# Kernel tuning notes

Measured on AMD Instinct MI355X. Metric: run time of the kernel, lower is better.

Reference implementation:

```python
import jax, jax.numpy as jnp
import numpy as np

N = 50000       # nodes
E = 800000      # edges (before self-loops)
F_IN = 128
HID = 64
HEADS = 4
OUT_DIM = 128
N_CLS = 2
NG = 500        # num graphs
SLOPE = 0.2     # GATConv leaky_relu negative slope
EPS = 1e-5      # BatchNorm eps


def setup_inputs() -> dict:
    key = jax.random.key(0)
    ks = jax.random.split(key, 24)
    s = 0.05
    d = {
        "x": jax.random.normal(ks[0], (N, F_IN), jnp.float32),
        "edge_index": jax.random.randint(ks[1], (2, E), 0, N, jnp.int64),
        "batch": jnp.sort(jax.random.randint(ks[2], (N,), 0, NG, jnp.int64)),
        # GATConv 1
        "W1": jax.random.normal(ks[3], (F_IN, HEADS * HID), jnp.float32) * s,
        "att_src1": jax.random.normal(ks[4], (HEADS, HID), jnp.float32) * s,
        "att_dst1": jax.random.normal(ks[5], (HEADS, HID), jnp.float32) * s,
        "b1": jnp.zeros((HEADS * HID,), jnp.float32),
        # BN1 (eval mode)
        "g1": jnp.ones((HEADS * HID,), jnp.float32),
        "be1": jnp.zeros((HEADS * HID,), jnp.float32),
        "rm1": jnp.zeros((HEADS * HID,), jnp.float32),
        "rv1": jnp.ones((HEADS * HID,), jnp.float32),
        # GATConv 2
        "W2": jax.random.normal(ks[6], (HEADS * HID, HEADS * HID), jnp.float32) * s,
        "att_src2": jax.random.normal(ks[7], (HEADS, HID), jnp.float32) * s,
        "att_dst2": jax.random.normal(ks[8], (HEADS, HID), jnp.float32) * s,
        "b2": jnp.zeros((HEADS * HID,), jnp.float32),
        # BN2 (eval mode)
        "g2": jnp.ones((HEADS * HID,), jnp.float32),
        "be2": jnp.zeros((HEADS * HID,), jnp.float32),
        "rm2": jnp.zeros((HEADS * HID,), jnp.float32),
        "rv2": jnp.ones((HEADS * HID,), jnp.float32),
        # MLP head
        "lw1": jax.random.normal(ks[9], (HEADS * HID, OUT_DIM), jnp.float32) * s,
        "lb1": jnp.zeros((OUT_DIM,), jnp.float32),
        "lw2": jax.random.normal(ks[10], (OUT_DIM, N_CLS), jnp.float32) * s,
        "lb2": jnp.zeros((N_CLS,), jnp.float32),
    }
    return d


def _gat_conv(x, src, dst, W, a_src, a_dst, b):
    """PyG GATConv (concat heads, add_self_loops=True, eval -> no dropout)."""
    n = x.shape[0]
    h = (x @ W).reshape(n, HEADS, -1)            # [N, H, C]
    loop = jnp.arange(n)
    s = jnp.concatenate([src, loop])             # self-loops appended
    d = jnp.concatenate([dst, loop])
    a_s = jnp.sum(h * a_src, axis=-1)            # [N, H]
    a_d = jnp.sum(h * a_dst, axis=-1)            # [N, H]
    e = jax.nn.leaky_relu(a_s[s] + a_d[d], SLOPE)   # [Et, H]
    # softmax over incoming edges per destination node
    m = jax.ops.segment_max(e, d, num_segments=n)
    ex = jnp.exp(e - m[d])
    denom = jax.ops.segment_sum(ex, d, num_segments=n)
    alpha = ex / denom[d]                        # [Et, H]
    msg = h[s] * alpha[:, :, None]               # [Et, H, C]
    out = jax.ops.segment_sum(msg, d, num_segments=n)
    return out.reshape(n, -1) + b


def _bn_eval(x, g, be, rm, rv):
    return (x - rm) * jax.lax.rsqrt(rv + EPS) * g + be


def reference(x, edge_index, batch, W1, att_src1, att_dst1, b1, g1, be1, rm1, rv1,
              W2, att_src2, att_dst2, b2, g2, be2, rm2, rv2, lw1, lb1, lw2, lb2):
    src, dst = edge_index[0], edge_index[1]
    h = jax.nn.relu(_gat_conv(x, src, dst, W1, att_src1, att_dst1, b1))
    h = _bn_eval(h, g1, be1, rm1, rv1)
    h = jax.nn.relu(_gat_conv(h, src, dst, W2, att_src2, att_dst2, b2))
    h = _bn_eval(h, g2, be2, rm2, rv2)
    # global mean pool over graphs
    sums = jax.ops.segment_sum(h, batch, num_segments=NG)
    cnt = jax.ops.segment_sum(jnp.ones((h.shape[0],), h.dtype), batch, num_segments=NG)
    pooled = sums / jnp.clip(cnt, 1.0)[:, None]
    z = jax.nn.relu(pooled @ lw1 + lb1)
    return z @ lw2 + lb2
```

## Files before the change

kernel.cpp:

```cpp
#include <hip/hip_runtime.h>
#include <hip/hip_bf16.h>
#include <math.h>

#define N_NODES 50000
#define M_PAD   50048
#define N_EDGES 800000
#define F_IN 128
#define HID 64
#define HEADS 4
#define FEAT 256
#define OUT_DIM 128
#define N_CLS 2
#define NG 500
#define SLOPE 0.2f
#define BN_EPS 1e-5f
#define WCAP 64
#define NCHUNK ((N_NODES + 255) / 256)

typedef __attribute__((ext_vector_type(8))) short short8;
typedef __attribute__((ext_vector_type(4))) float floatx4;
typedef __attribute__((ext_vector_type(2))) float floatx2;

__device__ inline unsigned short f2bf(float f) {
    unsigned int u = __float_as_uint(f);
    unsigned int lsb = (u >> 16) & 1u;
    return (unsigned short)((u + 0x7fffu + lsb) >> 16);
}

template<bool AF32>
__global__ __launch_bounds__(256, 2) void gemm_mfma_gat(
    const void* __restrict__ Av, const unsigned short* __restrict__ BT,
    const float* __restrict__ att_src, const float* __restrict__ att_dst,
    unsigned char* __restrict__ h8, float* __restrict__ a_s,
    float* __restrict__ a_d, int K) {
    constexpr int LS = 40;
    constexpr int C8 = 272;
    __shared__ __align__(16) unsigned char smem_raw[128 * C8];
    unsigned short* As = (unsigned short*)smem_raw;
    unsigned short* Bs = As + 128 * LS;
    unsigned char*  s8 = smem_raw;
    int t = threadIdx.x;
    int lane = t & 63, w = t >> 6;
    int row0 = blockIdx.x * 128;
    int mrow = lane & 15, quad = lane >> 4;

    floatx4 acc[8][4] = {};

    int rA = t >> 2, cA = (t & 3) * 8;

    const unsigned short* Ab = (const unsigned short*)Av;
    const float* Af = (const float*)Av;

    for (int k0 = 0; k0 < K; k0 += 32) {
        #pragma unroll
        for (int j = 0; j < 2; j++) {
            int r = rA + j * 64;
            if (AF32) {
                uint4 pk = make_uint4(0, 0, 0, 0);
                if (row0 + r < N_NODES) {
                    float4 f0 = *(const float4*)&Af[(long long)(row0 + r) * K + k0 + cA];
                    float4 f1 = *(const float4*)&Af[(long long)(row0 + r) * K + k0 + cA + 4];
                    pk.x = (unsigned)f2bf(f0.x) | ((unsigned)f2bf(f0.y) << 16);
                    pk.y = (unsigned)f2bf(f0.z) | ((unsigned)f2bf(f0.w) << 16);
                    pk.z = (unsigned)f2bf(f1.x) | ((unsigned)f2bf(f1.y) << 16);
                    pk.w = (unsigned)f2bf(f1.z) | ((unsigned)f2bf(f1.w) << 16);
                }
                *(uint4*)&As[r * LS + cA] = pk;
            } else {
                *(uint4*)&As[r * LS + cA] = *(const uint4*)&Ab[(long long)(row0 + r) * K + k0 + cA];
            }
        }
        #pragma unroll
        for (int j = 0; j < 4; j++) {
            int r = rA + j * 64;
            *(uint4*)&Bs[r * LS + cA] = *(const uint4*)&BT[(long long)r * K + k0 + cA];
        }
        __syncthreads();
        short8 bf[4];
        #pragma unroll
        for (int ni = 0; ni < 4; ni++)
            bf[ni] = *(const short8*)&Bs[(w * 64 + ni * 16 + mrow) * LS + quad * 8];
        #pragma unroll
        for (int mi = 0; mi < 8; mi++) {
            short8 af = *(const short8*)&As[(mi * 16 + mrow) * LS + quad * 8];
            #pragma unroll
            for (int ni = 0; ni < 4; ni++)
                acc[mi][ni] = __builtin_amdgcn_mfma_f32_16x16x32_bf16(af, bf[ni],
                                                                      acc[mi][ni], 0, 0, 0);
        }
        __syncthreads();
    }

    float ats[4], atd[4];
    #pragma unroll
    for (int ni = 0; ni < 4; ni++) {
        ats[ni] = att_src[w * 64 + ni * 16 + mrow];
        atd[ni] = att_dst[w * 64 + ni * 16 + mrow];
    }
    #pragma unroll
    for (int mi = 0; mi < 8; mi++) {
        #pragma unroll
        for (int r = 0; r < 4; r++) {
            int row = row0 + mi * 16 + quad * 4 + r;
            float ps = 0.f, pd = 0.f;
            #pragma unroll
            for (int ni = 0; ni < 4; ni++) {
                float v = acc[mi][ni][r];
                ps += v * ats[ni];
                pd += v * atd[ni];
            }
            #pragma unroll
            for (int off = 1; off < 16; off <<= 1) {
                ps += __shfl_xor(ps, off);
                pd += __shfl_xor(pd, off);
            }
            if (mrow == 0 && row < N_NODES) {
                a_s[row * 4 + w] = ps;
                a_d[row * 4 + w] = pd;
            }
        }
    }

    #pragma unroll
    for (int mi = 0; mi < 8; mi++)
        #pragma unroll
        for (int r = 0; r < 4; r++) {
            int row = mi * 16 + quad * 4 + r;
            #pragma unroll
            for (int ni = 0; ni < 4; ni += 2) {
                int pk = __builtin_amdgcn_cvt_pk_fp8_f32(acc[mi][ni][r],
                                                         acc[mi][ni + 1][r], 0, false);
                s8[row * C8 + w * 64 + ni * 16 + mrow]       = (unsigned char)(pk & 0xff);
                s8[row * C8 + w * 64 + (ni + 1) * 16 + mrow] = (unsigned char)((pk >> 8) & 0xff);
            }
        }
    __syncthreads();
    {
        int r2 = t >> 1, half = t & 1;
        const uint4* sp = (const uint4*)&s8[r2 * C8 + half * 128];
        uint4* dp = (uint4*)&h8[(long long)(row0 + r2) * FEAT + half * 128];
        #pragma unroll
        for (int k = 0; k < 8; k++)
            dp[k] = sp[k];
    }
}

__global__ void prep(const float* __restrict__ W1, const float* __restrict__ W2,
                     unsigned short* __restrict__ W1T, unsigned short* __restrict__ W2T,
                     int* __restrict__ deg, unsigned long long* __restrict__ h1bf_pad) {
    int i = blockIdx.x * 256 + threadIdx.x;
    if (i < F_IN * 256) {
        int k = i >> 8, n = i & 255;
        W1T[n * F_IN + k] = f2bf(W1[i]);
    }
    int j = i - F_IN * 256;
    if (j >= 0 && j < FEAT * 256) {
        int k = j >> 8, n = j & 255;
        W2T[n * FEAT + k] = f2bf(W2[j]);
    }
    if (i < N_NODES) deg[i] = 0;
    if (i < (M_PAD - N_NODES) * FEAT / 4) h1bf_pad[i] = 0ULL;
}

__global__ void degree_count(const int* __restrict__ src, const int* __restrict__ dst,
                             int* __restrict__ deg, int* __restrict__ epos) {
    int e = blockIdx.x * blockDim.x + threadIdx.x;
    if (e >= N_EDGES + N_NODES) return;
    int d = (e < N_EDGES) ? dst[e] : (e - N_EDGES);
    epos[e] = atomicAdd(&deg[d], 1);
}

__global__ __launch_bounds__(256) void scan_k1(const int* __restrict__ deg,
                                               int* __restrict__ bsum) {
    int b = blockIdx.x, t = threadIdx.x;
    int i = b * 256 + t;
    int v = (i < N_NODES) ? deg[i] : 0;
    #pragma unroll
    for (int off = 32; off > 0; off >>= 1) v += __shfl_down(v, off);
    __shared__ int ws[4];
    if ((t & 63) == 0) ws[t >> 6] = v;
    __syncthreads();
    if (t == 0) bsum[b] = ws[0] + ws[1] + ws[2] + ws[3];
}

__global__ __launch_bounds__(256) void scan_k2(const int* __restrict__ bsum,
                                               int* __restrict__ boff,
                                               int* __restrict__ row_start) {
    int t = threadIdx.x;
    int lane = t & 63, wid = t >> 6;
    int v = (t < NCHUNK) ? bsum[t] : 0;
    int x = v;
    #pragma unroll
    for (int off = 1; off < 64; off <<= 1) {
        int y = __shfl_up(x, off);
        if (lane >= off) x += y;
    }
    __shared__ int wsum[4], woff[4];
    if (lane == 63) wsum[wid] = x;
    __syncthreads();
    if (t == 0) {
        int s = 0;
        #pragma unroll
        for (int w = 0; w < 4; w++) { int tw = wsum[w]; woff[w] = s; s += tw; }
        row_start[N_NODES] = s;
    }
    __syncthreads();
    if (t < NCHUNK) boff[t] = x - v + woff[wid];
}

__global__ __launch_bounds__(256) void scan_k3(const int* __restrict__ deg,
                                               const int* __restrict__ boff,
                                               int* __restrict__ row_start) {
    int b = blockIdx.x, t = threadIdx.x;
    int lane = t & 63, wid = t >> 6;
    int i = b * 256 + t;
    int v = (i < N_NODES) ? deg[i] : 0;
    int x = v;
    #pragma unroll
    for (int off = 1; off < 64; off <<= 1) {
        int y = __shfl_up(x, off);
        if (lane >= off) x += y;
    }
    __shared__ int wsum[4], woff[4];
    if (lane == 63) wsum[wid] = x;
    __syncthreads();
    if (t == 0) {
        int s = boff[b];
        #pragma unroll
        for (int w = 0; w < 4; w++) { int tw = wsum[w]; woff[w] = s; s += tw; }
    }
    __syncthreads();
    if (i < N_NODES) row_start[i] = x - v + woff[wid];
}

__global__ void scatter_edges(const int* __restrict__ src, const int* __restrict__ dst,
                              const int* __restrict__ row_start, const int* __restrict__ epos,
                              int* __restrict__ csr_src) {
    int e = blockIdx.x * blockDim.x + threadIdx.x;
    if (e >= N_EDGES + N_NODES) return;
    int s, d;
    if (e < N_EDGES) { s = src[e]; d = dst[e]; } else { s = d = e - N_EDGES; }
    csr_src[row_start[d] + epos[e]] = s;
}

__global__ __launch_bounds__(256) void gat_fused(
    const int* __restrict__ row_start, const int* __restrict__ csr_src,
    const float* __restrict__ a_s, const float* __restrict__ a_d,
    const unsigned char* __restrict__ h8, const float* __restrict__ bias,
    const float* __restrict__ g, const float* __restrict__ be,
    const float* __restrict__ rm, const float* __restrict__ rv,
    unsigned short* __restrict__ out16) {
    int t = threadIdx.x;
    int lane = t & 63;
    int w = t >> 6;
    int hd = lane >> 4;
    int d = blockIdx.x * 4 + w;

    __shared__ float p_lds[4 * WCAP * 4];
    __shared__ int   o_lds[4 * WCAP];
    float* pw = &p_lds[w * WCAP * 4];
    int*   ow = &o_lds[w * WCAP];

    const unsigned int* __restrict__ H1 = (const unsigned int*)h8;

    int rs = row_start[d], re = row_start[d + 1];
    int deg = re - rs;
    float4 ad4 = *(const float4*)&a_d[d * 4];

    float den = 0.f;
    float4 acc = make_float4(0.f, 0.f, 0.f, 0.f);

    if (deg <= WCAP) {
        float lg[4] = {-INFINITY, -INFINITY, -INFINITY, -INFINITY};
        if (lane < deg) {
            int s = csr_src[rs + lane];
            ow[lane] = s * 64;
            float4 as4 = *(const float4*)&a_s[s * 4];
            float e0 = as4.x + ad4.x; lg[0] = e0 > 0.f ? e0 : SLOPE * e0;
            float e1 = as4.y + ad4.y; lg[1] = e1 > 0.f ? e1 : SLOPE * e1;
            float e2 = as4.z + ad4.z; lg[2] = e2 > 0.f ? e2 : SLOPE * e2;
            float e3 = as4.w + ad4.w; lg[3] = e3 > 0.f ? e3 : SLOPE * e3;
        }
        float mm = fmaxf(fmaxf(lg[0], lg[1]), fmaxf(lg[2], lg[3]));
        #pragma unroll
        for (int off = 1; off < 64; off <<= 1) mm = fmaxf(mm, __shfl_xor(mm, off));
        if (lane < deg) {
            float4 pq;
            pq.x = __expf(lg[0] - mm);
            pq.y = __expf(lg[1] - mm);
            pq.z = __expf(lg[2] - mm);
            pq.w = __expf(lg[3] - mm);
            *(float4*)&pw[lane * 4] = pq;
        }
        int e = 0;
        for (; e + 1 < deg; e += 2) {
            int oA = ow[e], oB = ow[e + 1];
            float pA = pw[e * 4 + hd], pB = pw[(e + 1) * 4 + hd];
            int uA = (int)H1[oA + lane];
            int uB = (int)H1[oB + lane];
            den += pA + pB;
            floatx2 a0 = __builtin_amdgcn_cvt_pk_f32_fp8(uA, false);
            floatx2 a1 = __builtin_amdgcn_cvt_pk_f32_fp8(uA, true);
            floatx2 b0 = __builtin_amdgcn_cvt_pk_f32_fp8(uB, false);
            floatx2 b1 = __builtin_amdgcn_cvt_pk_f32_fp8(uB, true);
            acc.x += pA * a0.x; acc.y += pA * a0.y;
            acc.z += pA * a1.x; acc.w += pA * a1.y;
            acc.x += pB * b0.x; acc.y += pB * b0.y;
            acc.z += pB * b1.x; acc.w += pB * b1.y;
        }
        if (e < deg) {
            int oA = ow[e];
            float pA = pw[e * 4 + hd];
            int uA = (int)H1[oA + lane];
            den += pA;
            floatx2 a0 = __builtin_amdgcn_cvt_pk_f32_fp8(uA, false);
            floatx2 a1 = __builtin_amdgcn_cvt_pk_f32_fp8(uA, true);
            acc.x += pA * a0.x; acc.y += pA * a0.y;
            acc.z += pA * a1.x; acc.w += pA * a1.y;
        }
    } else {
        float m_old = -INFINITY;
        for (int base = 0; base < deg; base += WCAP) {
            int cl = min(WCAP, deg - base);
            float lg[4] = {-INFINITY, -INFINITY, -INFINITY, -INFINITY};
            if (lane < cl) {
                int s = csr_src[rs + base + lane];
                ow[lane] = s * 64;
                float4 as4 = *(const float4*)&a_s[s * 4];
                float e0 = as4.x + ad4.x; lg[0] = e0 > 0.f ? e0 : SLOPE * e0;
                float e1 = as4.y + ad4.y; lg[1] = e1 > 0.f ? e1 : SLOPE * e1;
                float e2 = as4.z + ad4.z; lg[2] = e2 > 0.f ? e2 : SLOPE * e2;
                float e3 = as4.w + ad4.w; lg[3] = e3 > 0.f ? e3 : SLOPE * e3;
            }
            float mm = fmaxf(fmaxf(lg[0], lg[1]), fmaxf(lg[2], lg[3]));
            #pragma unroll
            for (int off = 1; off < 64; off <<= 1) mm = fmaxf(mm, __shfl_xor(mm, off));
            float m_new = fmaxf(m_old, mm);
            float alpha = __expf(m_old - m_new);
            m_old = m_new;
            if (lane < cl) {
                float4 pq;
                pq.x = __expf(lg[0] - m_new);
                pq.y = __expf(lg[1] - m_new);
                pq.z = __expf(lg[2] - m_new);
                pq.w = __expf(lg[3] - m_new);
                *(float4*)&pw[lane * 4] = pq;
            }
            acc.x *= alpha; acc.y *= alpha; acc.z *= alpha; acc.w *= alpha;
            den *= alpha;
            int e = 0;
            for (; e + 1 < cl; e += 2) {
                int oA = ow[e], oB = ow[e + 1];
                float pA = pw[e * 4 + hd], pB = pw[(e + 1) * 4 + hd];
                int uA = (int)H1[oA + lane];
                int uB = (int)H1[oB + lane];
                den += pA + pB;
                floatx2 a0 = __builtin_amdgcn_cvt_pk_f32_fp8(uA, false);
                floatx2 a1 = __builtin_amdgcn_cvt_pk_f32_fp8(uA, true);
                floatx2 b0 = __builtin_amdgcn_cvt_pk_f32_fp8(uB, false);
                floatx2 b1 = __builtin_amdgcn_cvt_pk_f32_fp8(uB, true);
                acc.x += pA * a0.x; acc.y += pA * a0.y;
                acc.z += pA * a1.x; acc.w += pA * a1.y;
                acc.x += pB * b0.x; acc.y += pB * b0.y;
                acc.z += pB * b1.x; acc.w += pB * b1.y;
            }
            if (e < cl) {
                int oA = ow[e];
                float pA = pw[e * 4 + hd];
                int uA = (int)H1[oA + lane];
                den += pA;
                floatx2 a0 = __builtin_amdgcn_cvt_pk_f32_fp8(uA, false);
                floatx2 a1 = __builtin_amdgcn_cvt_pk_f32_fp8(uA, true);
                acc.x += pA * a0.x; acc.y += pA * a0.y;
                acc.z += pA * a1.x; acc.w += pA * a1.y;
            }
        }
    }
    float inv = 1.f / den;
    int c0 = lane * 4;
    float4 bi = *(const float4*)&bias[c0];
    float4 gg = *(const float4*)&g[c0];
    float4 bb = *(const float4*)&be[c0];
    float4 mm4 = *(const float4*)&rm[c0];
    float4 vv = *(const float4*)&rv[c0];
    float v0 = fmaxf(acc.x * inv + bi.x, 0.f);
    float v1 = fmaxf(acc.y * inv + bi.y, 0.f);
    float v2 = fmaxf(acc.z * inv + bi.z, 0.f);
    float v3 = fmaxf(acc.w * inv + bi.w, 0.f);
    v0 = (v0 - mm4.x) * rsqrtf(vv.x + BN_EPS) * gg.x + bb.x;
    v1 = (v1 - mm4.y) * rsqrtf(vv.y + BN_EPS) * gg.y + bb.y;
    v2 = (v2 - mm4.z) * rsqrtf(vv.z + BN_EPS) * gg.z + bb.z;
    v3 = (v3 - mm4.w) * rsqrtf(vv.w + BN_EPS) * gg.w + bb.w;
    unsigned long long o =
        (unsigned long long)f2bf(v0) |
        ((unsigned long long)f2bf(v1) << 16) |
        ((unsigned long long)f2bf(v2) << 32) |
        ((unsigned long long)f2bf(v3) << 48);
    __builtin_nontemporal_store(o, (unsigned long long*)&out16[(long long)d * FEAT + c0]);
}

__global__ __launch_bounds__(256) void head_fused(
    const unsigned short* __restrict__ h2, const int* __restrict__ batch,
    const float* __restrict__ lw1, const float* __restrict__ lb1,
    const float* __restrict__ lw2, const float* __restrict__ lb2,
    float* __restrict__ out) {
    int gph = blockIdx.x;
    int t = threadIdx.x;
    __shared__ float pooled[FEAT];
    __shared__ float zl[OUT_DIM];
    __shared__ int lo_s, hi_s;
    if (t == 0) {
        int lo = 0, hi = N_NODES;
        while (lo < hi) { int mid = (lo + hi) >> 1; if (batch[mid] < gph) lo = mid + 1; else hi = mid; }
        lo_s = lo;
        int lo2 = 0, hi2 = N_NODES;
        while (lo2 < hi2) { int mid = (lo2 + hi2) >> 1; if (batch[mid] < gph + 1) lo2 = mid + 1; else hi2 = mid; }
        hi_s = lo2;
    }
    __syncthreads();
    int lo = lo_s, hi = hi_s;
    float a0 = 0.f, a1 = 0.f, a2 = 0.f, a3 = 0.f;
    int n = lo;
    for (; n + 3 < hi; n += 4) {
        a0 += __uint_as_float((unsigned)h2[(long long)n * FEAT + t] << 16);
        a1 += __uint_as_float((unsigned)h2[(long long)(n + 1) * FEAT + t] << 16);
        a2 += __uint_as_float((unsigned)h2[(long long)(n + 2) * FEAT + t] << 16);
        a3 += __uint_as_float((unsigned)h2[(long long)(n + 3) * FEAT + t] << 16);
    }
    for (; n < hi; n++) a0 += __uint_as_float((unsigned)h2[(long long)n * FEAT + t] << 16);
    float cnt = fmaxf((float)(hi - lo), 1.f);
    pooled[t] = (a0 + a1 + a2 + a3) / cnt;
    __syncthreads();
    int j = t >> 1, kh = t & 1;
    float zp = 0.f;
    #pragma unroll 8
    for (int k = kh * 128; k < kh * 128 + 128; k++)
        zp += pooled[k] * lw1[k * OUT_DIM + j];
    zp += __shfl_xor(zp, 1);
    if (kh == 0) zl[j] = fmaxf(zp + lb1[j], 0.f);
    __syncthreads();
    int w = t >> 6, lane = t & 63;
    if (w < 2) {
        float p = zl[lane] * lw2[lane * 2 + w] + zl[lane + 64] * lw2[(lane + 64) * 2 + w];
        #pragma unroll
        for (int off = 1; off < 64; off <<= 1) p += __shfl_xor(p, off);
        if (lane == 0) out[gph * 2 + w] = p + lb2[w];
    }
}

extern "C" void kernel_launch(void* const* d_in, const int* in_sizes, int n_in,
                              void* d_out, int out_size, void* d_ws, size_t ws_size,
                              hipStream_t stream) {
    const float* x       = (const float*)d_in[0];
    const int*   ei      = (const int*)d_in[1];
    const int*   batch   = (const int*)d_in[2];
    const float* W1      = (const float*)d_in[3];
    const float* att_s1  = (const float*)d_in[4];
    const float* att_d1  = (const float*)d_in[5];
    const float* b1      = (const float*)d_in[6];
    const float* g1      = (const float*)d_in[7];
    const float* be1     = (const float*)d_in[8];
    const float* rm1     = (const float*)d_in[9];
    const float* rv1     = (const float*)d_in[10];
    const float* W2      = (const float*)d_in[11];
    const float* att_s2  = (const float*)d_in[12];
    const float* att_d2  = (const float*)d_in[13];
    const float* b2      = (const float*)d_in[14];
    const float* g2      = (const float*)d_in[15];
    const float* be2     = (const float*)d_in[16];
    const float* rm2     = (const float*)d_in[17];
    const float* rv2     = (const float*)d_in[18];
    const float* lw1     = (const float*)d_in[19];
    const float* lb1     = (const float*)d_in[20];
    const float* lw2     = (const float*)d_in[21];
    const float* lb2     = (const float*)d_in[22];
    float* out           = (float*)d_out;

    const int* src = ei;
    const int* dst = ei + N_EDGES;

    char* p = (char*)d_ws;
    auto carve = [&p](size_t bytes) -> void* {
        void* r = (void*)p;
        p += (bytes + 63) & ~(size_t)63;
        return r;
    };
    unsigned short* h2bf = (unsigned short*)carve(sizeof(short) * (size_t)N_NODES * FEAT);
    float* a_s    = (float*)carve(sizeof(float) * N_NODES * HEADS);
    float* a_d    = (float*)carve(sizeof(float) * N_NODES * HEADS);
    int*   deg    = (int*)carve(sizeof(int) * N_NODES);
    int*   epos   = (int*)carve(sizeof(int) * (N_EDGES + N_NODES));
    int*   csr    = (int*)carve(sizeof(int) * (N_EDGES + N_NODES));
    int*   rstart = (int*)carve(sizeof(int) * (N_NODES + 4));
    int*   bsum   = (int*)carve(sizeof(int) * 256);
    int*   boff   = (int*)carve(sizeof(int) * 256);
    unsigned char*  h8   = (unsigned char*)carve((size_t)M_PAD * FEAT);
    unsigned short* h1bf = (unsigned short*)carve(sizeof(short) * (size_t)M_PAD * FEAT);
    unsigned short* w1t  = (unsigned short*)carve(sizeof(short) * FEAT * F_IN);
    unsigned short* w2t  = (unsigned short*)carve(sizeof(short) * FEAT * FEAT);

    const int Et = N_EDGES + N_NODES;

    prep<<<((F_IN + FEAT) * 256 + 255) / 256, 256, 0, stream>>>(
        W1, W2, w1t, w2t, deg,
        (unsigned long long*)(h1bf + (size_t)N_NODES * FEAT));

    degree_count<<<(Et + 255) / 256, 256, 0, stream>>>(src, dst, deg, epos);
    scan_k1<<<NCHUNK, 256, 0, stream>>>(deg, bsum);
    scan_k2<<<1, 256, 0, stream>>>(bsum, boff, rstart);
    scan_k3<<<NCHUNK, 256, 0, stream>>>(deg, boff, rstart);
    scatter_edges<<<(Et + 255) / 256, 256, 0, stream>>>(src, dst, rstart, epos, csr);

    gemm_mfma_gat<true><<<M_PAD / 128, 256, 0, stream>>>(x, w1t, att_s1, att_d1,
                                                         h8, a_s, a_d, F_IN);
    gat_fused<<<N_NODES / 4, 256, 0, stream>>>(rstart, csr, a_s, a_d, h8,
                                               b1, g1, be1, rm1, rv1, h1bf);

    gemm_mfma_gat<false><<<M_PAD / 128, 256, 0, stream>>>(h1bf, w2t, att_s2, att_d2,
                                                          h8, a_s, a_d, FEAT);
    gat_fused<<<N_NODES / 4, 256, 0, stream>>>(rstart, csr, a_s, a_d, h8,
                                               b2, g2, be2, rm2, rv2, h2bf);

    head_fused<<<NG, 256, 0, stream>>>(h2bf, batch, lw1, lb1, lw2, lb2, out);
}
```

Measured before the change: 339.9 us.

## Replace CSR build with ELL adjacency plus global overflow list

Replaces the degree-count, three-pass scan and scatter kernels with a single build_ell kernel. It writes each edge's source into a fixed 64-slot-per-node ELL table via atomic position, and spills edges beyond 64 into a global overflow list. The aggregation kernel reads the ELL row directly. For nodes with more than 64 edges it processes the 64 slots, then scans the whole overflow list with an online softmax. This removes four launches and the scan passes, but ELL writes are scattered and the overflow scan is linear in overflow size for every high-degree node.

Measured after the change: 322.4 us. -5.2%, faster.

```diff
diff --git a/kernel.cpp b/kernel.cpp
--- a/kernel.cpp
+++ b/kernel.cpp
@@ -14,8 +14,7 @@
 #define NG 500
 #define SLOPE 0.2f
 #define BN_EPS 1e-5f
-#define WCAP 64
-#define NCHUNK ((N_NODES + 255) / 256)
+#define ECAP 64
 
 typedef __attribute__((ext_vector_type(8))) short short8;
 typedef __attribute__((ext_vector_type(4))) float floatx4;
@@ -147,7 +146,8 @@
 
 __global__ void prep(const float* __restrict__ W1, const float* __restrict__ W2,
                      unsigned short* __restrict__ W1T, unsigned short* __restrict__ W2T,
-                     int* __restrict__ deg, unsigned long long* __restrict__ h1bf_pad) {
+                     int* __restrict__ deg, int* __restrict__ ovf_cnt,
+                     unsigned long long* __restrict__ h1bf_pad) {
     int i = blockIdx.x * 256 + threadIdx.x;
     if (i < F_IN * 256) {
         int k = i >> 8, n = i & 255;
@@ -159,92 +159,30 @@
         W2T[n * FEAT + k] = f2bf(W2[j]);
     }
     if (i < N_NODES) deg[i] = 0;
+    if (i == 0) *ovf_cnt = 0;
     if (i < (M_PAD - N_NODES) * FEAT / 4) h1bf_pad[i] = 0ULL;
 }
 
-__global__ void degree_count(const int* __restrict__ src, const int* __restrict__ dst,
-                             int* __restrict__ deg, int* __restrict__ epos) {
-    int e = blockIdx.x * blockDim.x + threadIdx.x;
-    if (e >= N_EDGES + N_NODES) return;
-    int d = (e < N_EDGES) ? dst[e] : (e - N_EDGES);
-    epos[e] = atomicAdd(&deg[d], 1);
-}
-
-__global__ __launch_bounds__(256) void scan_k1(const int* __restrict__ deg,
-                                               int* __restrict__ bsum) {
-    int b = blockIdx.x, t = threadIdx.x;
-    int i = b * 256 + t;
-    int v = (i < N_NODES) ? deg[i] : 0;
-    #pragma unroll
-    for (int off = 32; off > 0; off >>= 1) v += __shfl_down(v, off);
-    __shared__ int ws[4];
-    if ((t & 63) == 0) ws[t >> 6] = v;
-    __syncthreads();
-    if (t == 0) bsum[b] = ws[0] + ws[1] + ws[2] + ws[3];
-}
-
-__global__ __launch_bounds__(256) void scan_k2(const int* __restrict__ bsum,
-                                               int* __restrict__ boff,
-                                               int* __restrict__ row_start) {
-    int t = threadIdx.x;
-    int lane = t & 63, wid = t >> 6;
-    int v = (t < NCHUNK) ? bsum[t] : 0;
-    int x = v;
-    #pragma unroll
-    for (int off = 1; off < 64; off <<= 1) {
-        int y = __shfl_up(x, off);
-        if (lane >= off) x += y;
-    }
-    __shared__ int wsum[4], woff[4];
-    if (lane == 63) wsum[wid] = x;
-    __syncthreads();
-    if (t == 0) {
-        int s = 0;
-        #pragma unroll
-        for (int w = 0; w < 4; w++) { int tw = wsum[w]; woff[w] = s; s += tw; }
-        row_start[N_NODES] = s;
-    }
-    __syncthreads();
-    if (t < NCHUNK) boff[t] = x - v + woff[wid];
-}
-
-__global__ __launch_bounds__(256) void scan_k3(const int* __restrict__ deg,
-                                               const int* __restrict__ boff,
-                                               int* __restrict__ row_start) {
-    int b = blockIdx.x, t = threadIdx.x;
-    int lane = t & 63, wid = t >> 6;
-    int i = b * 256 + t;
-    int v = (i < N_NODES) ? deg[i] : 0;
-    int x = v;
-    #pragma unroll
-    for (int off = 1; off < 64; off <<= 1) {
-        int y = __shfl_up(x, off);
-        if (lane >= off) x += y;
-    }
-    __shared__ int wsum[4], woff[4];
-    if (lane == 63) wsum[wid] = x;
-    __syncthreads();
-    if (t == 0) {
-        int s = boff[b];
-        #pragma unroll
-        for (int w = 0; w < 4; w++) { int tw = wsum[w]; woff[w] = s; s += tw; }
-    }
-    __syncthreads();
-    if (i < N_NODES) row_start[i] = x - v + woff[wid];
-}
-
-__global__ void scatter_edges(const int* __restrict__ src, const int* __restrict__ dst,
-                              const int* __restrict__ row_start, const int* __restrict__ epos,
-                              int* __restrict__ csr_src) {
+__global__ void build_ell(const int* __restrict__ src, const int* __restrict__ dst,
+                          int* __restrict__ deg, int* __restrict__ ell,
+                          int* __restrict__ ovf_cnt, int* __restrict__ ovf) {
     int e = blockIdx.x * blockDim.x + threadIdx.x;
     if (e >= N_EDGES + N_NODES) return;
     int s, d;
     if (e < N_EDGES) { s = src[e]; d = dst[e]; } else { s = d = e - N_EDGES; }
-    csr_src[row_start[d] + epos[e]] = s;
+    int pos = atomicAdd(&deg[d], 1);
+    if (pos < ECAP) {
+        ell[d * ECAP + pos] = s;
+    } else {
+        int j = atomicAdd(ovf_cnt, 1);
+        ovf[2 * j] = s;
+        ovf[2 * j + 1] = d;
+    }
 }
 
 __global__ __launch_bounds__(256) void gat_fused(
-    const int* __restrict__ row_start, const int* __restrict__ csr_src,
+    const int* __restrict__ deg_arr, const int* __restrict__ ell,
+    const int* __restrict__ ovf_cnt, const int* __restrict__ ovf,
     const float* __restrict__ a_s, const float* __restrict__ a_d,
     const unsigned char* __restrict__ h8, const float* __restrict__ bias,
     const float* __restrict__ g, const float* __restrict__ be,
@@ -256,24 +194,23 @@
     int hd = lane >> 4;
     int d = blockIdx.x * 4 + w;
 
-    __shared__ float p_lds[4 * WCAP * 4];
-    __shared__ int   o_lds[4 * WCAP];
-    float* pw = &p_lds[w * WCAP * 4];
-    int*   ow = &o_lds[w * WCAP];
+    __shared__ float p_lds[4 * ECAP * 4];
+    __shared__ int   o_lds[4 * ECAP];
+    float* pw = &p_lds[w * ECAP * 4];
+    int*   ow = &o_lds[w * ECAP];
 
     const unsigned int* __restrict__ H1 = (const unsigned int*)h8;
 
-    int rs = row_start[d], re = row_start[d + 1];
-    int deg = re - rs;
+    int deg = deg_arr[d];
     float4 ad4 = *(const float4*)&a_d[d * 4];
 
     float den = 0.f;
     float4 acc = make_float4(0.f, 0.f, 0.f, 0.f);
 
-    if (deg <= WCAP) {
+    if (deg <= ECAP) {
         float lg[4] = {-INFINITY, -INFINITY, -INFINITY, -INFINITY};
         if (lane < deg) {
-            int s = csr_src[rs + lane];
+            int s = ell[d * ECAP + lane];
             ow[lane] = s * 64;
             float4 as4 = *(const float4*)&a_s[s * 4];
             float e0 = as4.x + ad4.x; lg[0] = e0 > 0.f ? e0 : SLOPE * e0;
@@ -319,52 +256,27 @@
             acc.z += pA * a1.x; acc.w += pA * a1.y;
         }
     } else {
-        float m_old = -INFINITY;
-        for (int base = 0; base < deg; base += WCAP) {
-            int cl = min(WCAP, deg - base);
-            float lg[4] = {-INFINITY, -INFINITY, -INFINITY, -INFINITY};
-            if (lane < cl) {
-                int s = csr_src[rs + base + lane];
-                ow[lane] = s * 64;
-                float4 as4 = *(const float4*)&a_s[s * 4];
-                float e0 = as4.x + ad4.x; lg[0] = e0 > 0.f ? e0 : SLOPE * e0;
-                float e1 = as4.y + ad4.y; lg[1] = e1 > 0.f ? e1 : SLOPE * e1;
-                float e2 = as4.z + ad4.z; lg[2] = e2 > 0.f ? e2 : SLOPE * e2;
-                float e3 = as4.w + ad4.w; lg[3] = e3 > 0.f ? e3 : SLOPE * e3;
-            }
+        float m_old;
+        {
+            int s = ell[d * ECAP + lane];
+            ow[lane] = s * 64;
+            float4 as4 = *(const float4*)&a_s[s * 4];
+            float lg[4];
+            float e0 = as4.x + ad4.x; lg[0] = e0 > 0.f ? e0 : SLOPE * e0;
+            float e1 = as4.y + ad4.y; lg[1] = e1 > 0.f ? e1 : SLOPE * e1;
+            float e2 = as4.z + ad4.z; lg[2] = e2 > 0.f ? e2 : SLOPE * e2;
+            float e3 = as4.w + ad4.w; lg[3] = e3 > 0.f ? e3 : SLOPE * e3;
             float mm = fmaxf(fmaxf(lg[0], lg[1]), fmaxf(lg[2], lg[3]));
             #pragma unroll
             for (int off = 1; off < 64; off <<= 1) mm = fmaxf(mm, __shfl_xor(mm, off));
-            float m_new = fmaxf(m_old, mm);
-            float alpha = __expf(m_old - m_new);
-            m_old = m_new;
-            if (lane < cl) {
-                float4 pq;
-                pq.x = __expf(lg[0] - m_new);
-                pq.y = __expf(lg[1] - m_new);
-                pq.z = __expf(lg[2] - m_new);
-                pq.w = __expf(lg[3] - m_new);
-                *(float4*)&pw[lane * 4] = pq;
-            }
-            acc.x *= alpha; acc.y *= alpha; acc.z *= alpha; acc.w *= alpha;
-            den *= alpha;
-            int e = 0;
-            for (; e + 1 < cl; e += 2) {
-                int oA = ow[e], oB = ow[e + 1];
-                float pA = pw[e * 4 + hd], pB = pw[(e + 1) * 4 + hd];
-                int uA = (int)H1[oA + lane];
-                int uB = (int)H1[oB + lane];
-                den += pA + pB;
-                floatx2 a0 = __builtin_amdgcn_cvt_pk_f32_fp8(uA, false);
-                floatx2 a1 = __builtin_amdgcn_cvt_pk_f32_fp8(uA, true);
-                floatx2 b0 = __builtin_amdgcn_cvt_pk_f32_fp8(uB, false);
-                floatx2 b1 = __builtin_amdgcn_cvt_pk_f32_fp8(uB, true);
-                acc.x += pA * a0.x; acc.y += pA * a0.y;
-                acc.z += pA * a1.x; acc.w += pA * a1.y;
-                acc.x += pB * b0.x; acc.y += pB * b0.y;
-                acc.z += pB * b1.x; acc.w += pB * b1.y;
-            }
-            if (e < cl) {
+            m_old = mm;
+            float4 pq;
+            pq.x = __expf(lg[0] - mm);
+            pq.y = __expf(lg[1] - mm);
+            pq.z = __expf(lg[2] - mm);
+            pq.w = __expf(lg[3] - mm);
+            *(float4*)&pw[lane * 4] = pq;
+            for (int e = 0; e < ECAP; e++) {
                 int oA = ow[e];
                 float pA = pw[e * 4 + hd];
                 int uA = (int)H1[oA + lane];
@@ -374,6 +286,29 @@
                 acc.x += pA * a0.x; acc.y += pA * a0.y;
                 acc.z += pA * a1.x; acc.w += pA * a1.y;
             }
+        }
+        int nov = *ovf_cnt;
+        for (int i = 0; i < nov; i++) {
+            int s2 = ovf[2 * i], d2 = ovf[2 * i + 1];
+            if (d2 != d) continue;
+            float4 as4 = *(const float4*)&a_s[s2 * 4];
+            float lg[4];
+            float e0 = as4.x + ad4.x; lg[0] = e0 > 0.f ? e0 : SLOPE * e0;
+            float e1 = as4.y + ad4.y; lg[1] = e1 > 0.f ? e1 : SLOPE * e1;
+            float e2 = as4.z + ad4.z; lg[2] = e2 > 0.f ? e2 : SLOPE * e2;
+            float e3 = as4.w + ad4.w; lg[3] = e3 > 0.f ? e3 : SLOPE * e3;
+            float mmax = fmaxf(fmaxf(lg[0], lg[1]), fmaxf(lg[2], lg[3]));
+            float m_new = fmaxf(m_old, mmax);
+            float alpha = __expf(m_old - m_new);
+            m_old = m_new;
+            float ph = __expf(lg[hd] - m_new);
+            acc.x *= alpha; acc.y *= alpha; acc.z *= alpha; acc.w *= alpha;
+            den = den * alpha + ph;
+            int u = (int)H1[s2 * 64 + lane];
+            floatx2 a0 = __builtin_amdgcn_cvt_pk_f32_fp8(u, false);
+            floatx2 a1 = __builtin_amdgcn_cvt_pk_f32_fp8(u, true);
+            acc.x += ph * a0.x; acc.y += ph * a0.y;
+            acc.z += ph * a1.x; acc.w += ph * a1.y;
         }
     }
     float inv = 1.f / den;
@@ -489,11 +424,9 @@
     float* a_s    = (float*)carve(sizeof(float) * N_NODES * HEADS);
     float* a_d    = (float*)carve(sizeof(float) * N_NODES * HEADS);
     int*   deg    = (int*)carve(sizeof(int) * N_NODES);
-    int*   epos   = (int*)carve(sizeof(int) * (N_EDGES + N_NODES));
-    int*   csr    = (int*)carve(sizeof(int) * (N_EDGES + N_NODES));
-    int*   rstart = (int*)carve(sizeof(int) * (N_NODES + 4));
-    int*   bsum   = (int*)carve(sizeof(int) * 256);
-    int*   boff   = (int*)carve(sizeof(int) * 256);
+    int*   ell    = (int*)carve(sizeof(int) * (size_t)N_NODES * ECAP);
+    int*   ovf_cnt= (int*)carve(sizeof(int) * 16);
+    int*   ovf    = (int*)carve(sizeof(int) * 2 * (N_EDGES + N_NODES));
     unsigned char*  h8   = (unsigned char*)carve((size_t)M_PAD * FEAT);
     unsigned short* h1bf = (unsigned short*)carve(sizeof(short) * (size_t)M_PAD * FEAT);
     unsigned short* w1t  = (unsigned short*)carve(sizeof(short) * FEAT * F_IN);
@@ -502,23 +435,19 @@
     const int Et = N_EDGES + N_NODES;
 
     prep<<<((F_IN + FEAT) * 256 + 255) / 256, 256, 0, stream>>>(
-        W1, W2, w1t, w2t, deg,
+        W1, W2, w1t, w2t, deg, ovf_cnt,
         (unsigned long long*)(h1bf + (size_t)N_NODES * FEAT));
 
-    degree_count<<<(Et + 255) / 256, 256, 0, stream>>>(src, dst, deg, epos);
-    scan_k1<<<NCHUNK, 256, 0, stream>>>(deg, bsum);
-    scan_k2<<<1, 256, 0, stream>>>(bsum, boff, rstart);
-    scan_k3<<<NCHUNK, 256, 0, stream>>>(deg, boff, rstart);
-    scatter_edges<<<(Et + 255) / 256, 256, 0, stream>>>(src, dst, rstart, epos, csr);
+    build_ell<<<(Et + 255) / 256, 256, 0, stream>>>(src, dst, deg, ell, ovf_cnt, ovf);
 
     gemm_mfma_gat<true><<<M_PAD / 128, 256, 0, stream>>>(x, w1t, att_s1, att_d1,
                                                          h8, a_s, a_d, F_IN);
-    gat_fused<<<N_NODES / 4, 256, 0, stream>>>(rstart, csr, a_s, a_d, h8,
+    gat_fused<<<N_NODES / 4, 256, 0, stream>>>(deg, ell, ovf_cnt, ovf, a_s, a_d, h8,
                                                b1, g1, be1, rm1, rv1, h1bf);
 
     gemm_mfma_gat<false><<<M_PAD / 128, 256, 0, stream>>>(h1bf, w2t, att_s2, att_d2,
                                                           h8, a_s, a_d, FEAT);
-    gat_fused<<<N_NODES / 4, 256, 0, stream>>>(rstart, csr, a_s, a_d, h8,
+    gat_fused<<<N_NODES / 4, 256, 0, stream>>>(deg, ell, ovf_cnt, ovf, a_s, a_d, h8,
                                                b2, g2, be2, rm2, rv2, h2bf);
 
     head_fused<<<NG, 256, 0, stream>>>(h2bf, batch, lw1, lb1, lw2, lb2, out);
```
